# Kernel optimization log

Hardware: AMD Instinct MI355X
Metric: run time of the kernel (lower is better)

The kernel has to match this reference:

```python
import jax, jax.numpy as jnp
import numpy as np

N_HEAD = 16
N_KV_HEAD = 4
N_EMBD = 2048

def rotate_half(x):
    x1, x2 = jnp.split(x, 2, axis=-1)
    return jnp.concatenate([-x2, x1], axis=-1)

def rope_tables(T, k):
    # angles = 10000^(-2*i/k) for i in [0, k/2); cos/sin repeated twice along last dim
    inv = jnp.power(10000.0, -2.0 * jnp.arange(k // 2, dtype=jnp.float32) / k)
    ang = jnp.arange(T, dtype=jnp.float32)[:, None] * inv[None, :]  # [T, k/2]
    cos = jnp.tile(jnp.cos(ang), (1, 2))  # [T, k]
    sin = jnp.tile(jnp.sin(ang), (1, 2))
    return cos, sin

def setup_inputs() -> dict:
    key = jax.random.key(0)
    ks = jax.random.split(key, 5)
    B, T, D = 4, 1024, N_EMBD
    g, h = N_KV_HEAD, N_HEAD
    k = D // h
    s = 0.02
    return {
        'x': jax.random.normal(ks[0], (B, T, D), dtype=jnp.float32),
        'Wq': jax.random.normal(ks[1], (D, D), dtype=jnp.float32) * s,
        'Wk': jax.random.normal(ks[2], (D, g * k), dtype=jnp.float32) * s,
        'Wv': jax.random.normal(ks[3], (D, g * k), dtype=jnp.float32) * s,
        'Wo': jax.random.normal(ks[4], (D, D), dtype=jnp.float32) * s,
    }

def reference(x, Wq, Wk, Wv, Wo):
    B, T, D = x.shape
    h, g = N_HEAD, N_KV_HEAD
    k = D // h
    Q = (x @ Wq).reshape(B, T, h, k).transpose(0, 2, 1, 3)  # [B,h,T,k]
    K = (x @ Wk).reshape(B, T, g, k).transpose(0, 2, 1, 3)  # [B,g,T,k]
    V = (x @ Wv).reshape(B, T, g, k).transpose(0, 2, 1, 3)
    # GQA: repeat_interleave kv heads to match query heads
    K = jnp.repeat(K, h // g, axis=1)  # [B,h,T,k]
    V = jnp.repeat(V, h // g, axis=1)
    cos, sin = rope_tables(T, k)
    cos = cos[None, None]  # [1,1,T,k]
    sin = sin[None, None]
    Q = Q * cos + rotate_half(Q) * sin
    K = K * cos + rotate_half(K) * sin
    scores = jnp.einsum('bhqk,bhsk->bhqs', Q, K) / jnp.sqrt(jnp.float32(k))
    causal = jnp.tril(jnp.ones((T, T), dtype=bool))
    scores = jnp.where(causal[None, None], scores, -jnp.inf)
    A = jax.nn.softmax(scores, axis=-1)
    Y = jnp.einsum('bhqs,bhsk->bhqk', A, V)
    Y = Y.transpose(0, 2, 1, 3).reshape(B, T, D)
    return Y @ Wo
```

## Files before the change

kernel.cpp:

```cpp
#include <hip/hip_runtime.h>
#include <math.h>

#define B_ 4
#define T_ 1024
#define D_ 2048
#define NH 16
#define NKV 4
#define HD 128
#define KV_D 512
#define QKV_W 3072

typedef __attribute__((ext_vector_type(8))) short short8;
typedef __attribute__((ext_vector_type(4))) float f32x4;

__device__ __forceinline__ ushort f2b(float f) {
    unsigned u = __float_as_uint(f);
    return (ushort)((u + 0x7fffu + ((u >> 16) & 1u)) >> 16);
}
__device__ __forceinline__ float b2f(ushort u) {
    return __uint_as_float((unsigned)u << 16);
}

#if __has_builtin(__builtin_amdgcn_exp2f)
#define EXP2F(x) __builtin_amdgcn_exp2f(x)
#else
#define EXP2F(x) __expf((x) * 0.6931471805599453f)
#endif

#define ASYNC_COPY16(g, l)                                                  \
    __builtin_amdgcn_global_load_lds(                                       \
        (const __attribute__((address_space(1))) void*)(g),                 \
        (__attribute__((address_space(3))) void*)(l), 16, 0, 0)

__global__ __launch_bounds__(256) void prep_all(const float* __restrict__ x,
                                                const float* __restrict__ Wq,
                                                const float* __restrict__ Wk,
                                                const float* __restrict__ Wv,
                                                const float* __restrict__ Wo,
                                                ushort* __restrict__ xb,
                                                ushort* __restrict__ WqkvT,
                                                ushort* __restrict__ WoT) {
    __shared__ float tile[32][33];
    const int bid = blockIdx.x;
    if (bid < 8192) {
        const int i = bid * 256 + threadIdx.x;
        const float4 v = ((const float4*)x)[i];
        ushort4 u;
        u.x = f2b(v.x); u.y = f2b(v.y); u.z = f2b(v.z); u.w = f2b(v.w);
        ((ushort4*)xb)[i] = u;
        return;
    }
    const float* W;
    ushort* WT;
    int N, rb;
    if (bid < 12288)      { W = Wq; WT = WqkvT;                           N = D_;   rb = bid - 8192; }
    else if (bid < 13312) { W = Wk; WT = WqkvT + (size_t)D_ * D_;         N = KV_D; rb = bid - 12288; }
    else if (bid < 14336) { W = Wv; WT = WqkvT + (size_t)(D_+KV_D) * D_;  N = KV_D; rb = bid - 13312; }
    else                  { W = Wo; WT = WoT;                             N = D_;   rb = bid - 14336; }
    const int bxn = N / 32;
    const int n0 = (rb % bxn) * 32, k0 = (rb / bxn) * 32;
    const int tx = threadIdx.x & 31, ty = threadIdx.x >> 5;
    for (int i = ty; i < 32; i += 8)
        tile[i][tx] = W[(size_t)(k0 + i) * N + n0 + tx];
    __syncthreads();
    for (int i = ty; i < 32; i += 8)
        WT[(size_t)(n0 + i) * D_ + k0 + tx] = f2b(tile[tx][i]);
}

template <bool OUT_BF16>
__global__ __launch_bounds__(256) void gemm_bf16_t(const ushort* __restrict__ A,
                                                   const ushort* __restrict__ BT,
                                                   void* __restrict__ Cv,
                                                   int M, int N, int K) {
    __shared__ ushort As[128 * 32];
    __shared__ ushort Bs[128 * 32];
    const int tid = threadIdx.x;
    const int m0 = blockIdx.y * 128, n0 = blockIdx.x * 128;
    const int wave = tid >> 6, lane = tid & 63;
    const int wm = (wave >> 1) * 64, wn = (wave & 1) * 64;
    const int lrow = lane & 15;
    const int quad = lane >> 4;

    f32x4 acc[4][4];
    const f32x4 zero = {0.f, 0.f, 0.f, 0.f};
#pragma unroll
    for (int i = 0; i < 4; ++i)
#pragma unroll
        for (int j = 0; j < 4; ++j) acc[i][j] = zero;

    const int srow = tid >> 2;
    const int scol = (tid & 3) * 8;
    const ushort* Ag = A + (size_t)(m0 + srow) * K + scol;
    const ushort* Bg = BT + (size_t)(n0 + srow) * K + scol;
    ushort* AsT = As + tid * 8;
    ushort* BsT = Bs + tid * 8;

    for (int k0 = 0; k0 < K; k0 += 32) {
        ASYNC_COPY16(Ag + k0, AsT);
        ASYNC_COPY16(Ag + k0 + (size_t)64 * K, AsT + 64 * 32);
        ASYNC_COPY16(Bg + k0, BsT);
        ASYNC_COPY16(Bg + k0 + (size_t)64 * K, BsT + 64 * 32);
        __syncthreads();

        short8 a[4], b[4];
#pragma unroll
        for (int mt = 0; mt < 4; ++mt)
            a[mt] = *(const short8*)&As[(wm + mt * 16 + lrow) * 32 + quad * 8];
#pragma unroll
        for (int nt = 0; nt < 4; ++nt)
            b[nt] = *(const short8*)&Bs[(wn + nt * 16 + lrow) * 32 + quad * 8];
#pragma unroll
        for (int mt = 0; mt < 4; ++mt)
#pragma unroll
            for (int nt = 0; nt < 4; ++nt)
                acc[mt][nt] = __builtin_amdgcn_mfma_f32_16x16x32_bf16(
                    a[mt], b[nt], acc[mt][nt], 0, 0, 0);
        __syncthreads();
    }

    const int crow = quad * 4;
    const int ccol = lrow;
#pragma unroll
    for (int mt = 0; mt < 4; ++mt)
#pragma unroll
        for (int nt = 0; nt < 4; ++nt)
#pragma unroll
            for (int r = 0; r < 4; ++r) {
                const size_t idx = (size_t)(m0 + wm + mt * 16 + crow + r) * N +
                                   n0 + wn + nt * 16 + ccol;
                if (OUT_BF16) ((ushort*)Cv)[idx] = f2b(acc[mt][nt][r]);
                else          ((float*)Cv)[idx] = acc[mt][nt][r];
            }
}

__global__ __launch_bounds__(256) void prep2(ushort* __restrict__ QKV,
                                             ushort* __restrict__ Vt) {
    __shared__ ushort tile[32][34];
    const int bid = blockIdx.x;
    if (bid < 20480) {
        const int idx = bid * 256 + threadIdx.x;
        const int i = idx & 63;
        const int tmp = idx >> 6;
        const int head = tmp % (NH + NKV);
        const int bt = tmp / (NH + NKV);
        const int t = bt & (T_ - 1);
        const float inv = exp2f((float)i * (-13.287712379549449f / 64.0f));
        const float ang = (float)t * inv;
        const float c = cosf(ang), s = sinf(ang);
        const bool isQ = head < NH;
        const size_t base = (size_t)bt * QKV_W +
                            (isQ ? head * HD : D_ + (head - NH) * HD);
        const float sc = isQ ? (0.08838834764831845f * 1.4426950408889634f) : 1.0f;
        const float x1 = b2f(QKV[base + i]);
        const float x2 = b2f(QKV[base + i + 64]);
        QKV[base + i]      = f2b((x1 * c - x2 * s) * sc);
        QKV[base + i + 64] = f2b((x2 * c + x1 * s) * sc);
        return;
    }
    const int b2 = bid - 20480;
    const int bkv = b2 >> 7;
    const int rem = b2 & 127;
    const int t0 = (rem >> 2) * 32, d0 = (rem & 3) * 32;
    const int b = bkv >> 2, kv = bkv & 3;
    const int tx = threadIdx.x & 31, ty = threadIdx.x >> 5;
    for (int i = ty; i < 32; i += 8)
        tile[i][tx] = QKV[(size_t)(b * T_ + t0 + i) * QKV_W + D_ + KV_D + kv * HD + d0 + tx];
    __syncthreads();
    for (int i = ty; i < 32; i += 8)
        Vt[((size_t)((b * NKV + kv) * HD + d0 + i)) * T_ + t0 + tx] = tile[tx][i];
}

__global__ __launch_bounds__(256) void attn_mfma(const ushort* __restrict__ QKV,
                                                 const ushort* __restrict__ Vt,
                                                 ushort* __restrict__ Yb) {
    __shared__ ushort Ks[64][136];
    __shared__ ushort Vs[128][72];
    __shared__ ushort Ps[4][16][72];

    const int bh = blockIdx.x;
    const int qt = (int)gridDim.y - 1 - (int)blockIdx.y;
    const int b = bh >> 4, h = bh & 15;
    const int kvh = h >> 2;
    const int q0 = qt * 64;
    const int tid = threadIdx.x;
    const int wave = tid >> 6, lane = tid & 63;
    const int ln = lane & 15, quad = lane >> 4;

    short8 qf[4];
    {
        const ushort* qp = QKV + ((size_t)(b * T_ + q0 + wave * 16 + ln)) * QKV_W + h * HD + quad * 8;
#pragma unroll
        for (int f = 0; f < 4; ++f) qf[f] = *(const short8*)(qp + f * 32);
    }

    f32x4 acc[8];
    const f32x4 zero = {0.f, 0.f, 0.f, 0.f};
#pragma unroll
    for (int j = 0; j < 8; ++j) acc[j] = zero;
    float m_r[4], l_r[4];
#pragma unroll
    for (int r = 0; r < 4; ++r) { m_r[r] = -INFINITY; l_r[r] = 0.f; }

    const int qrow = q0 + wave * 16 + quad * 4;

    for (int kt = 0; kt <= qt; ++kt) {
        const int s0 = kt * 64;
        __syncthreads();
#pragma unroll
        for (int c = 0; c < 4; ++c) {
            const int cid = tid + 256 * c;
            const int s = cid >> 4, ch = cid & 15;
            *(short8*)&Ks[s][ch * 8] =
                *(const short8*)&QKV[((size_t)(b * T_ + s0 + s)) * QKV_W + D_ + kvh * HD + ch * 8];
        }
#pragma unroll
        for (int c = 0; c < 4; ++c) {
            const int cid = tid + 256 * c;
            const int d = cid >> 3, ch = cid & 7;
            *(short8*)&Vs[d][ch * 8] =
                *(const short8*)&Vt[((size_t)((b * NKV + kvh) * HD + d)) * T_ + s0 + ch * 8];
        }
        __syncthreads();

        float sc[4][4];
#pragma unroll
        for (int ct = 0; ct < 4; ++ct) {
            f32x4 s4 = zero;
#pragma unroll
            for (int f = 0; f < 4; ++f)
                s4 = __builtin_amdgcn_mfma_f32_16x16x32_bf16(
                    qf[f], *(const short8*)&Ks[ct * 16 + ln][f * 32 + quad * 8], s4, 0, 0, 0);
#pragma unroll
            for (int r = 0; r < 4; ++r) sc[ct][r] = s4[r];
        }
        if (kt == qt) {
#pragma unroll
            for (int ct = 0; ct < 4; ++ct)
#pragma unroll
                for (int r = 0; r < 4; ++r)
                    if (s0 + ct * 16 + ln > qrow + r) sc[ct][r] = -INFINITY;
        }
        float alpha[4];
#pragma unroll
        for (int r = 0; r < 4; ++r) {
            float mx = fmaxf(fmaxf(sc[0][r], sc[1][r]), fmaxf(sc[2][r], sc[3][r]));
            mx = fmaxf(mx, __shfl_xor(mx, 1));
            mx = fmaxf(mx, __shfl_xor(mx, 2));
            mx = fmaxf(mx, __shfl_xor(mx, 4));
            mx = fmaxf(mx, __shfl_xor(mx, 8));
            const float mnew = fmaxf(m_r[r], mx);
            alpha[r] = EXP2F(m_r[r] - mnew);
            m_r[r] = mnew;
#pragma unroll
            for (int ct = 0; ct < 4; ++ct) sc[ct][r] = EXP2F(sc[ct][r] - mnew);
            float sum = (sc[0][r] + sc[1][r]) + (sc[2][r] + sc[3][r]);
            sum += __shfl_xor(sum, 1);
            sum += __shfl_xor(sum, 2);
            sum += __shfl_xor(sum, 4);
            sum += __shfl_xor(sum, 8);
            l_r[r] = l_r[r] * alpha[r] + sum;
        }
#pragma unroll
        for (int ct = 0; ct < 4; ++ct)
#pragma unroll
            for (int r = 0; r < 4; ++r)
                Ps[wave][quad * 4 + r][ct * 16 + ln] = f2b(sc[ct][r]);
#pragma unroll
        for (int j = 0; j < 8; ++j)
#pragma unroll
            for (int r = 0; r < 4; ++r) acc[j][r] *= alpha[r];
        const short8 pa0 = *(const short8*)&Ps[wave][ln][quad * 8];
        const short8 pa1 = *(const short8*)&Ps[wave][ln][32 + quad * 8];
#pragma unroll
        for (int j = 0; j < 8; ++j) {
            acc[j] = __builtin_amdgcn_mfma_f32_16x16x32_bf16(
                pa0, *(const short8*)&Vs[j * 16 + ln][quad * 8], acc[j], 0, 0, 0);
            acc[j] = __builtin_amdgcn_mfma_f32_16x16x32_bf16(
                pa1, *(const short8*)&Vs[j * 16 + ln][32 + quad * 8], acc[j], 0, 0, 0);
        }
    }

    float invl[4];
#pragma unroll
    for (int r = 0; r < 4; ++r) invl[r] = 1.f / l_r[r];
    ushort* yb = Yb + ((size_t)(b * T_ + qrow)) * D_ + h * HD + ln;
#pragma unroll
    for (int r = 0; r < 4; ++r)
#pragma unroll
        for (int j = 0; j < 8; ++j)
            yb[(size_t)r * D_ + j * 16] = f2b(acc[j][r] * invl[r]);
}

extern "C" void kernel_launch(void* const* d_in, const int* in_sizes, int n_in,
                              void* d_out, int out_size, void* d_ws, size_t ws_size,
                              hipStream_t stream) {
    const float* x  = (const float*)d_in[0];
    const float* Wq = (const float*)d_in[1];
    const float* Wk = (const float*)d_in[2];
    const float* Wv = (const float*)d_in[3];
    const float* Wo = (const float*)d_in[4];
    float* out = (float*)d_out;

    char* w = (char*)d_ws;
    ushort* xb    = (ushort*)w;  w += (size_t)4096 * D_ * 2;
    ushort* WqkvT = (ushort*)w;  w += (size_t)QKV_W * D_ * 2;
    ushort* QKV   = (ushort*)w;  w += (size_t)4096 * QKV_W * 2;
    ushort* Vt    = (ushort*)w;  w += (size_t)B_ * KV_D * T_ * 2;
    ushort* Yb    = (ushort*)w;  w += (size_t)4096 * D_ * 2;
    ushort* WoT   = (ushort*)w;  w += (size_t)D_ * D_ * 2;

    const int M = B_ * T_;
    dim3 blk(256);

    prep_all<<<18432, blk, 0, stream>>>(x, Wq, Wk, Wv, Wo, xb, WqkvT, WoT);

    gemm_bf16_t<true><<<dim3(QKV_W / 128, M / 128), blk, 0, stream>>>(
        xb, WqkvT, QKV, M, QKV_W, D_);

    prep2<<<22528, blk, 0, stream>>>(QKV, Vt);

    attn_mfma<<<dim3(B_ * NH, T_ / 64), blk, 0, stream>>>(QKV, Vt, Yb);

    gemm_bf16_t<false><<<dim3(D_ / 128, M / 128), blk, 0, stream>>>(
        Yb, WoT, out, M, D_, D_);
}
```

Before: 312.8 us.

## Fuse RoPE, scaling and V transpose into the QKV GEMM epilogue

The QKV projection GEMM now stages its output tile in shared memory and applies RoPE plus the query scaling, using a precomputed cos/sin table, before writing Q/K. The V tile is written straight into the transposed Vt layout, so the separate prep2 kernel and its read-modify-write pass over QKV are gone. The QKV buffer stride shrinks because V is no longer stored there. The cos/sin table is built inside the prep kernel. The trade-off is a heavier GEMM epilogue with extra shared-memory traffic and table loads.

```diff
diff --git a/kernel.cpp b/kernel.cpp
--- a/kernel.cpp
+++ b/kernel.cpp
@@ -8,7 +8,7 @@
 #define NKV 4
 #define HD 128
 #define KV_D 512
-#define QKV_W 3072
+#define QKV_S 2560
 
 typedef __attribute__((ext_vector_type(8))) short short8;
 typedef __attribute__((ext_vector_type(4))) float f32x4;
@@ -39,7 +39,8 @@
                                                 const float* __restrict__ Wo,
                                                 ushort* __restrict__ xb,
                                                 ushort* __restrict__ WqkvT,
-                                                ushort* __restrict__ WoT) {
+                                                ushort* __restrict__ WoT,
+                                                float2* __restrict__ tab) {
     __shared__ float tile[32][33];
     const int bid = blockIdx.x;
     if (bid < 8192) {
@@ -48,6 +49,14 @@
         ushort4 u;
         u.x = f2b(v.x); u.y = f2b(v.y); u.z = f2b(v.z); u.w = f2b(v.w);
         ((ushort4*)xb)[i] = u;
+        return;
+    }
+    if (bid >= 18432) {
+        const int idx = (bid - 18432) * 256 + threadIdx.x;
+        const int t = idx >> 6, i = idx & 63;
+        const float inv = exp2f((float)i * (-13.287712379549449f / 64.0f));
+        const float ang = (float)t * inv;
+        tab[idx] = make_float2(cosf(ang), sinf(ang));
         return;
     }
     const float* W;
@@ -67,11 +76,122 @@
         WT[(size_t)(n0 + i) * D_ + k0 + tx] = f2b(tile[tx][i]);
 }
 
-template <bool OUT_BF16>
-__global__ __launch_bounds__(256) void gemm_bf16_t(const ushort* __restrict__ A,
-                                                   const ushort* __restrict__ BT,
-                                                   void* __restrict__ Cv,
-                                                   int M, int N, int K) {
+__global__ __launch_bounds__(256) void gemm_qkv(const ushort* __restrict__ A,
+                                                const ushort* __restrict__ BT,
+                                                ushort* __restrict__ QKV,
+                                                ushort* __restrict__ Vt,
+                                                const float2* __restrict__ tab) {
+    __shared__ ushort smem[128 * 136];
+    ushort* As = smem;
+    ushort* Bs = smem + 4096;
+    const int K = D_;
+    const int tid = threadIdx.x;
+    const int m0 = blockIdx.y * 128, n0 = blockIdx.x * 128;
+    const int hid = n0 >> 7;
+    const int wave = tid >> 6, lane = tid & 63;
+    const int wm = (wave >> 1) * 64, wn = (wave & 1) * 64;
+    const int lrow = lane & 15;
+    const int quad = lane >> 4;
+
+    f32x4 acc[4][4];
+    const f32x4 zero = {0.f, 0.f, 0.f, 0.f};
+#pragma unroll
+    for (int i = 0; i < 4; ++i)
+#pragma unroll
+        for (int j = 0; j < 4; ++j) acc[i][j] = zero;
+
+    const int srow = tid >> 2;
+    const int scol = (tid & 3) * 8;
+    const ushort* Ag = A + (size_t)(m0 + srow) * K + scol;
+    const ushort* Bg = BT + (size_t)(n0 + srow) * K + scol;
+    ushort* AsT = As + tid * 8;
+    ushort* BsT = Bs + tid * 8;
+
+    for (int k0 = 0; k0 < K; k0 += 32) {
+        ASYNC_COPY16(Ag + k0, AsT);
+        ASYNC_COPY16(Ag + k0 + (size_t)64 * K, AsT + 64 * 32);
+        ASYNC_COPY16(Bg + k0, BsT);
+        ASYNC_COPY16(Bg + k0 + (size_t)64 * K, BsT + 64 * 32);
+        __syncthreads();
+
+        short8 a[4], b[4];
+#pragma unroll
+        for (int mt = 0; mt < 4; ++mt)
+            a[mt] = *(const short8*)&As[(wm + mt * 16 + lrow) * 32 + quad * 8];
+#pragma unroll
+        for (int nt = 0; nt < 4; ++nt)
+            b[nt] = *(const short8*)&Bs[(wn + nt * 16 + lrow) * 32 + quad * 8];
+#pragma unroll
+        for (int mt = 0; mt < 4; ++mt)
+#pragma unroll
+            for (int nt = 0; nt < 4; ++nt)
+                acc[mt][nt] = __builtin_amdgcn_mfma_f32_16x16x32_bf16(
+                    a[mt], b[nt], acc[mt][nt], 0, 0, 0);
+        __syncthreads();
+    }
+
+    ushort* Epi = smem;
+#pragma unroll
+    for (int mt = 0; mt < 4; ++mt)
+#pragma unroll
+        for (int nt = 0; nt < 4; ++nt)
+#pragma unroll
+            for (int r = 0; r < 4; ++r)
+                Epi[(wm + mt * 16 + quad * 4 + r) * 136 + wn + nt * 16 + lrow] =
+                    f2b(acc[mt][nt][r]);
+    __syncthreads();
+
+    const int b = m0 >> 10;
+    const int t0 = m0 & 1023;
+
+    if (hid < NH + NKV) {
+        const bool isQ = hid < NH;
+        const size_t colbase = isQ ? hid * HD : (size_t)D_ + (hid - NH) * HD;
+        const float sc = isQ ? (0.08838834764831845f * 1.4426950408889634f) : 1.0f;
+        const int r = tid >> 1;
+        const int hf = tid & 1;
+        const int t = t0 + r;
+        ushort* orow = QKV + (size_t)(m0 + r) * QKV_S + colbase;
+        const float4* tab4 = (const float4*)tab;
+#pragma unroll
+        for (int jj = 0; jj < 4; ++jj) {
+            const int dbase = hf * 32 + jj * 8;
+            const short8 lo = *(const short8*)&Epi[r * 136 + dbase];
+            const short8 hi = *(const short8*)&Epi[r * 136 + 64 + dbase];
+            ushort olo[8], ohi[8];
+#pragma unroll
+            for (int k = 0; k < 4; ++k) {
+                const float4 cs = tab4[((t * 64 + dbase) >> 1) + k];
+                const float x1a = b2f(lo[2 * k]),     x2a = b2f(hi[2 * k]);
+                const float x1b = b2f(lo[2 * k + 1]), x2b = b2f(hi[2 * k + 1]);
+                olo[2 * k]     = f2b((x1a * cs.x - x2a * cs.y) * sc);
+                ohi[2 * k]     = f2b((x2a * cs.x + x1a * cs.y) * sc);
+                olo[2 * k + 1] = f2b((x1b * cs.z - x2b * cs.w) * sc);
+                ohi[2 * k + 1] = f2b((x2b * cs.z + x1b * cs.w) * sc);
+            }
+            *(short8*)&orow[dbase]      = *(short8*)olo;
+            *(short8*)&orow[dbase + 64] = *(short8*)ohi;
+        }
+    } else {
+        const int kv = hid - (NH + NKV);
+        const int d = tid & 127;
+        const int hf = tid >> 7;
+        ushort* vrow = Vt + ((size_t)((b * NKV + kv) * HD + d)) * T_ + t0 + hf * 64;
+#pragma unroll
+        for (int jj = 0; jj < 8; ++jj) {
+            ushort pk[8];
+#pragma unroll
+            for (int k = 0; k < 8; ++k)
+                pk[k] = Epi[(hf * 64 + jj * 8 + k) * 136 + d];
+            *(short8*)&vrow[jj * 8] = *(short8*)pk;
+        }
+    }
+}
+
+__global__ __launch_bounds__(256) void gemm_bf16(const ushort* __restrict__ A,
+                                                 const ushort* __restrict__ BT,
+                                                 float* __restrict__ C,
+                                                 int M, int N, int K) {
     __shared__ ushort As[128 * 32];
     __shared__ ushort Bs[128 * 32];
     const int tid = threadIdx.x;
@@ -125,49 +245,9 @@
 #pragma unroll
         for (int nt = 0; nt < 4; ++nt)
 #pragma unroll
-            for (int r = 0; r < 4; ++r) {
-                const size_t idx = (size_t)(m0 + wm + mt * 16 + crow + r) * N +
-                                   n0 + wn + nt * 16 + ccol;
-                if (OUT_BF16) ((ushort*)Cv)[idx] = f2b(acc[mt][nt][r]);
-                else          ((float*)Cv)[idx] = acc[mt][nt][r];
-            }
-}
-
-__global__ __launch_bounds__(256) void prep2(ushort* __restrict__ QKV,
-                                             ushort* __restrict__ Vt) {
-    __shared__ ushort tile[32][34];
-    const int bid = blockIdx.x;
-    if (bid < 20480) {
-        const int idx = bid * 256 + threadIdx.x;
-        const int i = idx & 63;
-        const int tmp = idx >> 6;
-        const int head = tmp % (NH + NKV);
-        const int bt = tmp / (NH + NKV);
-        const int t = bt & (T_ - 1);
-        const float inv = exp2f((float)i * (-13.287712379549449f / 64.0f));
-        const float ang = (float)t * inv;
-        const float c = cosf(ang), s = sinf(ang);
-        const bool isQ = head < NH;
-        const size_t base = (size_t)bt * QKV_W +
-                            (isQ ? head * HD : D_ + (head - NH) * HD);
-        const float sc = isQ ? (0.08838834764831845f * 1.4426950408889634f) : 1.0f;
-        const float x1 = b2f(QKV[base + i]);
-        const float x2 = b2f(QKV[base + i + 64]);
-        QKV[base + i]      = f2b((x1 * c - x2 * s) * sc);
-        QKV[base + i + 64] = f2b((x2 * c + x1 * s) * sc);
-        return;
-    }
-    const int b2 = bid - 20480;
-    const int bkv = b2 >> 7;
-    const int rem = b2 & 127;
-    const int t0 = (rem >> 2) * 32, d0 = (rem & 3) * 32;
-    const int b = bkv >> 2, kv = bkv & 3;
-    const int tx = threadIdx.x & 31, ty = threadIdx.x >> 5;
-    for (int i = ty; i < 32; i += 8)
-        tile[i][tx] = QKV[(size_t)(b * T_ + t0 + i) * QKV_W + D_ + KV_D + kv * HD + d0 + tx];
-    __syncthreads();
-    for (int i = ty; i < 32; i += 8)
-        Vt[((size_t)((b * NKV + kv) * HD + d0 + i)) * T_ + t0 + tx] = tile[tx][i];
+            for (int r = 0; r < 4; ++r)
+                C[(size_t)(m0 + wm + mt * 16 + crow + r) * N +
+                  n0 + wn + nt * 16 + ccol] = acc[mt][nt][r];
 }
 
 __global__ __launch_bounds__(256) void attn_mfma(const ushort* __restrict__ QKV,
@@ -188,7 +268,7 @@
 
     short8 qf[4];
     {
-        const ushort* qp = QKV + ((size_t)(b * T_ + q0 + wave * 16 + ln)) * QKV_W + h * HD + quad * 8;
+        const ushort* qp = QKV + ((size_t)(b * T_ + q0 + wave * 16 + ln)) * QKV_S + h * HD + quad * 8;
 #pragma unroll
         for (int f = 0; f < 4; ++f) qf[f] = *(const short8*)(qp + f * 32);
     }
@@ -211,7 +291,7 @@
             const int cid = tid + 256 * c;
             const int s = cid >> 4, ch = cid & 15;
             *(short8*)&Ks[s][ch * 8] =
-                *(const short8*)&QKV[((size_t)(b * T_ + s0 + s)) * QKV_W + D_ + kvh * HD + ch * 8];
+                *(const short8*)&QKV[((size_t)(b * T_ + s0 + s)) * QKV_S + D_ + kvh * HD + ch * 8];
         }
 #pragma unroll
         for (int c = 0; c < 4; ++c) {
@@ -303,24 +383,21 @@
 
     char* w = (char*)d_ws;
     ushort* xb    = (ushort*)w;  w += (size_t)4096 * D_ * 2;
-    ushort* WqkvT = (ushort*)w;  w += (size_t)QKV_W * D_ * 2;
-    ushort* QKV   = (ushort*)w;  w += (size_t)4096 * QKV_W * 2;
+    ushort* WqkvT = (ushort*)w;  w += (size_t)3072 * D_ * 2;
+    ushort* QKV   = (ushort*)w;  w += (size_t)4096 * QKV_S * 2;
     ushort* Vt    = (ushort*)w;  w += (size_t)B_ * KV_D * T_ * 2;
     ushort* Yb    = (ushort*)w;  w += (size_t)4096 * D_ * 2;
     ushort* WoT   = (ushort*)w;  w += (size_t)D_ * D_ * 2;
+    float2* tab   = (float2*)w;  w += (size_t)T_ * 64 * 8;
 
     const int M = B_ * T_;
     dim3 blk(256);
 
-    prep_all<<<18432, blk, 0, stream>>>(x, Wq, Wk, Wv, Wo, xb, WqkvT, WoT);
-
-    gemm_bf16_t<true><<<dim3(QKV_W / 128, M / 128), blk, 0, stream>>>(
-        xb, WqkvT, QKV, M, QKV_W, D_);
-
-    prep2<<<22528, blk, 0, stream>>>(QKV, Vt);
+    prep_all<<<18688, blk, 0, stream>>>(x, Wq, Wk, Wv, Wo, xb, WqkvT, WoT, tab);
+
+    gemm_qkv<<<dim3(3072 / 128, M / 128), blk, 0, stream>>>(xb, WqkvT, QKV, Vt, tab);
 
     attn_mfma<<<dim3(B_ * NH, T_ / 64), blk, 0, stream>>>(QKV, Vt, Yb);
 
-    gemm_bf16_t<false><<<dim3(D_ / 128, M / 128), blk, 0, stream>>>(
-        Yb, WoT, out, M, D_, D_);
-}
+    gemm_bf16<<<dim3(D_ / 128, M / 128), blk, 0, stream>>>(Yb, WoT, out, M, D_, D_);
+}
```

New measurement: 297.7 us. 1.05x faster.
